# Kernel tuning notes

Measured on AMD Instinct MI355X. Metric: run time of the kernel, lower is better.

Reference implementation:

```python
import jax, jax.numpy as jnp
import numpy as np

B, D, N_LABELS = 8192, 512, 256

def setup_inputs() -> dict:
    key = jax.random.key(0)
    kz, km = jax.random.split(key)
    z = jax.random.normal(kz, (B, D), dtype=jnp.float32)
    Mx = jax.random.randint(km, (B,), 0, N_LABELS, dtype=jnp.int64)
    return {"z": z, "Mx": Mx}

def reference(z, Mx):
    # Mx: [B] int labels -> equality mask [B, B] with zero diagonal
    Mx2 = Mx.reshape(-1, 1)  # [B, 1]
    mask_Mx = (Mx2 == Mx2.T).astype(z.dtype)
    mask_Mx = mask_Mx * (1.0 - jnp.eye(z.shape[0], dtype=z.dtype))
    # pairwise L2 distances (cdist p=2) via gram trick, grad-safe sqrt
    sq = jnp.sum(z * z, axis=-1)                      # [B]
    d2 = sq[:, None] + sq[None, :] - 2.0 * (z @ z.T)  # [B, B]
    pos = d2 > 0.0
    dist = jnp.sqrt(jnp.where(pos, d2, 1.0)) * pos.astype(z.dtype)
    n_select = mask_Mx.sum(axis=1)                    # [B]
    valid = n_select > 0
    row_sum = (mask_Mx * dist).sum(axis=1)
    # torch masked_select drops rows with no positives; with these label
    # stats every row has positives, so returning the full [B] vector
    # (zeros where invalid) matches the selected result.
    loss = jnp.where(valid, row_sum / jnp.maximum(n_select, 1.0), 0.0)
    return loss
```

## Files before the change

kernel.cpp:

```cpp
#include <hip/hip_runtime.h>
#include <math.h>

#define B_ROWS 8192
#define D_DIM 512
#define N_LABELS 256
#define GMAX 64
#define THREADS 1024
#define WAVES 16
#define SEG (B_ROWS / WAVES)
#define SITER (SEG / 64)
#define LSTRIDE (D_DIM + 8)

typedef __attribute__((ext_vector_type(8))) _Float16 f16x8;
typedef __attribute__((ext_vector_type(4))) float f32x4;

static __device__ __forceinline__ unsigned short f2h(float f) {
    const _Float16 h = (_Float16)f;
    return __builtin_bit_cast(unsigned short, h);
}

__global__ __launch_bounds__(THREADS) void loss_kernel(const float* __restrict__ z,
                                                       const int* __restrict__ Mx,
                                                       float* __restrict__ out) {
    __shared__ __align__(16) unsigned short h_sh[GMAX][LSTRIDE];
    __shared__ int   ids_sh[GMAX];
    __shared__ float sq_sh[GMAX];
    __shared__ float rowpart[WAVES][GMAX];
    __shared__ unsigned long long msk_sh[WAVES][SITER];
    __shared__ int   wcnt[WAVES], wbase[WAVES];
    __shared__ int   cnt_sh;

    const int lbl  = blockIdx.x;
    const int tid  = threadIdx.x;
    const int wv   = tid >> 6;
    const int lane = tid & 63;
    const int sb   = wv * SEG;

    int c = 0;
    #pragma unroll
    for (int t = 0; t < SITER; ++t) {
        const bool m = (Mx[sb + t * 64 + lane] == lbl);
        const unsigned long long bal = __ballot(m);
        if (lane == 0) msk_sh[wv][t] = bal;
        c += __popcll(bal);
    }
    if (lane == 0) wcnt[wv] = c;
    __syncthreads();

    if (wv == 0) {
        int v = (lane < WAVES) ? wcnt[lane] : 0;
        #pragma unroll
        for (int d = 1; d < WAVES; d <<= 1) {
            const int o = __shfl_up(v, d, 64);
            if (lane >= d) v += o;
        }
        if (lane < WAVES) wbase[lane] = v - wcnt[lane];
        if (lane == WAVES - 1) cnt_sh = v;
    }
    __syncthreads();
    const int cnt = cnt_sh;
    if (cnt <= 0) return;

    if (cnt > GMAX) {
        int k = 0;
        for (int i = 0; i < B_ROWS; ++i) {
            if (Mx[i] != lbl) continue;
            if ((k++ % WAVES) != wv) continue;
            float acc = 0.f;
            for (int j = 0; j < B_ROWS; ++j) {
                if (Mx[j] != lbl || j == i) continue;
                float s = 0.f;
                for (int d = lane; d < D_DIM; d += 64) {
                    const float t = z[(size_t)i * D_DIM + d] - z[(size_t)j * D_DIM + d];
                    s = fmaf(t, t, s);
                }
                s += __shfl_xor(s, 1, 64);
                s += __shfl_xor(s, 2, 64);
                s += __shfl_xor(s, 4, 64);
                s += __shfl_xor(s, 8, 64);
                s += __shfl_xor(s, 16, 64);
                s += __shfl_xor(s, 32, 64);
                acc += (s > 0.f) ? sqrtf(s) : 0.f;
            }
            if (lane == 0) out[i] = acc / (float)(cnt - 1);
        }
        return;
    }

    {
        int pos = wbase[wv];
        const unsigned long long lower = (lane == 0) ? 0ull : ((1ull << lane) - 1ull);
        #pragma unroll
        for (int t = 0; t < SITER; ++t) {
            const unsigned long long bal = msk_sh[wv][t];
            if ((bal >> lane) & 1ull)
                ids_sh[pos + __popcll(bal & lower)] = sb + t * 64 + lane;
            pos += __popcll(bal);
        }
    }
    for (int i = tid; i < WAVES * GMAX; i += THREADS) ((float*)rowpart)[i] = 0.f;
    __syncthreads();

    for (int c2 = tid; c2 < cnt * (D_DIM / 4); c2 += THREADS) {
        const int row = c2 >> 7;
        const int c4  = c2 & 127;
        const float4 v = *(const float4*)(z + (size_t)ids_sh[row] * D_DIM + c4 * 4);
        const unsigned int p0 = (unsigned int)f2h(v.x) | ((unsigned int)f2h(v.y) << 16);
        const unsigned int p1 = (unsigned int)f2h(v.z) | ((unsigned int)f2h(v.w) << 16);
        *(uint2*)&h_sh[row][c4 * 4] = make_uint2(p0, p1);
    }
    __syncthreads();

    const int NT = (cnt + 15) >> 4;
    const int TS = NT * (NT + 1) / 2;

    int jt = 0;
    #pragma unroll
    for (int q = 1; q < 4; ++q) jt += (wv >= q * (q + 1) / 2);
    const int it = wv - jt * (jt + 1) / 2;
    const bool own = (wv < TS);

    const int l15 = lane & 15;
    const int lh  = lane >> 4;

    f32x4 acc = {0.f, 0.f, 0.f, 0.f};
    if (own) {
        #pragma unroll
        for (int k4 = 0; k4 < D_DIM / 32; ++k4) {
            const int kb = k4 * 32 + lh * 8;
            const f16x8 a = *(const f16x8*)&h_sh[it * 16 + l15][kb];
            const f16x8 b = *(const f16x8*)&h_sh[jt * 16 + l15][kb];
            acc = __builtin_amdgcn_mfma_f32_16x16x32_f16(a, b, acc, 0, 0, 0);
        }
    }

    if (own && it == jt) {
        #pragma unroll
        for (int r = 0; r < 4; ++r) {
            const int drow = lh * 4 + r;
            if (l15 == drow) sq_sh[it * 16 + drow] = acc[r];
        }
    }
    __syncthreads();

    if (own) {
        float d0 = 0.f, d1 = 0.f, d2v = 0.f, d3 = 0.f;
        #pragma unroll
        for (int r = 0; r < 4; ++r) {
            const int gi = it * 16 + lh * 4 + r;
            const int gj = jt * 16 + l15;
            const float d2 = sq_sh[gi] + sq_sh[gj] - 2.f * acc[r];
            const bool valid = (gi < cnt) && (gj < cnt) && (gi != gj) && (d2 > 0.f);
            const float dist = valid ? sqrtf(d2) : 0.f;
            if (r == 0) d0 = dist; else if (r == 1) d1 = dist; else if (r == 2) d2v = dist; else d3 = dist;

            float rs = dist;
            rs += __shfl_xor(rs, 1, 64);
            rs += __shfl_xor(rs, 2, 64);
            rs += __shfl_xor(rs, 4, 64);
            rs += __shfl_xor(rs, 8, 64);
            if (l15 == 0) rowpart[wv][gi] += rs;
        }
        if (it != jt) {
            float cs = (d0 + d1) + (d2v + d3);
            cs += __shfl_xor(cs, 16, 64);
            cs += __shfl_xor(cs, 32, 64);
            if (lane < 16) rowpart[wv][jt * 16 + l15] += cs;
        }
    }
    __syncthreads();

    if (tid < cnt) {
        float s = 0.f;
        #pragma unroll
        for (int w = 0; w < WAVES; ++w) s += rowpart[w][tid];
        out[ids_sh[tid]] = (cnt > 1) ? s / (float)(cnt - 1) : 0.f;
    }
}

extern "C" void kernel_launch(void* const* d_in, const int* in_sizes, int n_in,
                              void* d_out, int out_size, void* d_ws, size_t ws_size,
                              hipStream_t stream) {
    const float* z  = (const float*)d_in[0];
    const int*   Mx = (const int*)d_in[1];
    float*       out = (float*)d_out;

    loss_kernel<<<N_LABELS, THREADS, 0, stream>>>(z, Mx, out);
}
```

Baseline: 12.94 us.

## Fuse row gather with squared-norm computation per wave, dropping mask staging and barriers

Each wave now keeps its ballot masks in registers and gathers its own matching rows directly. One full wave loads each row, converts it to fp16, stores it to shared memory and computes the row's squared norm with a wave reduction. This removes the shared mask staging, one barrier before the gather, and the barrier that followed extracting norms from the diagonal MFMA tiles. In exchange, each wave processes its matching rows one after another, and a wave with many matches becomes the critical path.

```diff
diff --git a/kernel.cpp b/kernel.cpp
--- a/kernel.cpp
+++ b/kernel.cpp
@@ -18,6 +18,9 @@
     const _Float16 h = (_Float16)f;
     return __builtin_bit_cast(unsigned short, h);
 }
+static __device__ __forceinline__ float h2f(unsigned short u) {
+    return (float)__builtin_bit_cast(_Float16, u);
+}
 
 __global__ __launch_bounds__(THREADS) void loss_kernel(const float* __restrict__ z,
                                                        const int* __restrict__ Mx,
@@ -26,7 +29,6 @@
     __shared__ int   ids_sh[GMAX];
     __shared__ float sq_sh[GMAX];
     __shared__ float rowpart[WAVES][GMAX];
-    __shared__ unsigned long long msk_sh[WAVES][SITER];
     __shared__ int   wcnt[WAVES], wbase[WAVES];
     __shared__ int   cnt_sh;
 
@@ -36,15 +38,15 @@
     const int lane = tid & 63;
     const int sb   = wv * SEG;
 
+    unsigned long long bal[SITER];
     int c = 0;
     #pragma unroll
     for (int t = 0; t < SITER; ++t) {
-        const bool m = (Mx[sb + t * 64 + lane] == lbl);
-        const unsigned long long bal = __ballot(m);
-        if (lane == 0) msk_sh[wv][t] = bal;
-        c += __popcll(bal);
+        bal[t] = __ballot(Mx[sb + t * 64 + lane] == lbl);
+        c += __popcll(bal[t]);
     }
     if (lane == 0) wcnt[wv] = c;
+    for (int i = tid; i < WAVES * GMAX; i += THREADS) ((float*)rowpart)[i] = 0.f;
     __syncthreads();
 
     if (wv == 0) {
@@ -66,7 +68,7 @@
         for (int i = 0; i < B_ROWS; ++i) {
             if (Mx[i] != lbl) continue;
             if ((k++ % WAVES) != wv) continue;
-            float acc = 0.f;
+            float acc2 = 0.f;
             for (int j = 0; j < B_ROWS; ++j) {
                 if (Mx[j] != lbl || j == i) continue;
                 float s = 0.f;
@@ -80,34 +82,55 @@
                 s += __shfl_xor(s, 8, 64);
                 s += __shfl_xor(s, 16, 64);
                 s += __shfl_xor(s, 32, 64);
-                acc += (s > 0.f) ? sqrtf(s) : 0.f;
+                acc2 += (s > 0.f) ? sqrtf(s) : 0.f;
             }
-            if (lane == 0) out[i] = acc / (float)(cnt - 1);
+            if (lane == 0) out[i] = acc2 / (float)(cnt - 1);
         }
         return;
     }
 
     {
         int pos = wbase[wv];
-        const unsigned long long lower = (lane == 0) ? 0ull : ((1ull << lane) - 1ull);
         #pragma unroll
         for (int t = 0; t < SITER; ++t) {
-            const unsigned long long bal = msk_sh[wv][t];
-            if ((bal >> lane) & 1ull)
-                ids_sh[pos + __popcll(bal & lower)] = sb + t * 64 + lane;
-            pos += __popcll(bal);
-        }
-    }
-    for (int i = tid; i < WAVES * GMAX; i += THREADS) ((float*)rowpart)[i] = 0.f;
-    __syncthreads();
-
-    for (int c2 = tid; c2 < cnt * (D_DIM / 4); c2 += THREADS) {
-        const int row = c2 >> 7;
-        const int c4  = c2 & 127;
-        const float4 v = *(const float4*)(z + (size_t)ids_sh[row] * D_DIM + c4 * 4);
-        const unsigned int p0 = (unsigned int)f2h(v.x) | ((unsigned int)f2h(v.y) << 16);
-        const unsigned int p1 = (unsigned int)f2h(v.z) | ((unsigned int)f2h(v.w) << 16);
-        *(uint2*)&h_sh[row][c4 * 4] = make_uint2(p0, p1);
+            unsigned long long m = bal[t];
+            while (m) {
+                const int b = __ffsll((long long)m) - 1;
+                m &= m - 1;
+                const int row = sb + t * 64 + b;
+                const float* __restrict__ zp = z + (size_t)row * D_DIM + lane * 8;
+                const float4 v0 = *(const float4*)(zp);
+                const float4 v1 = *(const float4*)(zp + 4);
+                const unsigned short e0 = f2h(v0.x), e1 = f2h(v0.y), e2 = f2h(v0.z), e3 = f2h(v0.w);
+                const unsigned short e4 = f2h(v1.x), e5 = f2h(v1.y), e6 = f2h(v1.z), e7 = f2h(v1.w);
+                uint4 pk;
+                pk.x = (unsigned int)e0 | ((unsigned int)e1 << 16);
+                pk.y = (unsigned int)e2 | ((unsigned int)e3 << 16);
+                pk.z = (unsigned int)e4 | ((unsigned int)e5 << 16);
+                pk.w = (unsigned int)e6 | ((unsigned int)e7 << 16);
+                *(uint4*)&h_sh[pos][lane * 8] = pk;
+
+                float sp = h2f(e0) * h2f(e0);
+                sp = fmaf(h2f(e1), h2f(e1), sp);
+                sp = fmaf(h2f(e2), h2f(e2), sp);
+                sp = fmaf(h2f(e3), h2f(e3), sp);
+                sp = fmaf(h2f(e4), h2f(e4), sp);
+                sp = fmaf(h2f(e5), h2f(e5), sp);
+                sp = fmaf(h2f(e6), h2f(e6), sp);
+                sp = fmaf(h2f(e7), h2f(e7), sp);
+                sp += __shfl_xor(sp, 1, 64);
+                sp += __shfl_xor(sp, 2, 64);
+                sp += __shfl_xor(sp, 4, 64);
+                sp += __shfl_xor(sp, 8, 64);
+                sp += __shfl_xor(sp, 16, 64);
+                sp += __shfl_xor(sp, 32, 64);
+                if (lane == 0) {
+                    ids_sh[pos] = row;
+                    sq_sh[pos]  = sp;
+                }
+                ++pos;
+            }
+        }
     }
     __syncthreads();
 
@@ -133,15 +156,6 @@
             acc = __builtin_amdgcn_mfma_f32_16x16x32_f16(a, b, acc, 0, 0, 0);
         }
     }
-
-    if (own && it == jt) {
-        #pragma unroll
-        for (int r = 0; r < 4; ++r) {
-            const int drow = lh * 4 + r;
-            if (l15 == drow) sq_sh[it * 16 + drow] = acc[r];
-        }
-    }
-    __syncthreads();
 
     if (own) {
         float d0 = 0.f, d1 = 0.f, d2v = 0.f, d3 = 0.f;
```

Result: slower. 13.37 us (+3.3%).
